# Optimization experiments

Hardware: AMD Instinct MI355X
Metric: run time of the kernel (lower is better)

The kernel has to match this reference:

```python
import jax, jax.numpy as jnp
import numpy as np

DIM = 128; DSTATE = 64; DHEAD = 64; EXPAND = 2
DINNER = EXPAND * DIM; NH = DINNER // DHEAD
CONVK = 4; CHUNK = 128
BATCH = 1; DD = 32; HH = 32; WW = 32
CONVCH = DINNER + 2 * DSTATE
DPROJ = 2 * DINNER + 2 * DSTATE + NH


def rmsnorm(v, w, eps=1e-6):
    return v * jax.lax.rsqrt(jnp.mean(v * v, axis=-1, keepdims=True) + eps) * w


def ssd(xh, dt, A, Bm, Cm):
    # chunked SSD selective scan. xh [b,l,h,p], dt [b,l,h], A [h], Bm/Cm [b,l,n]
    b, l, h, p = xh.shape
    n = Bm.shape[-1]
    c, k = l // CHUNK, CHUNK
    dA = (dt * A).reshape(b, c, k, h)
    xdt = (xh * dt[..., None]).reshape(b, c, k, h, p)
    Bm = Bm.reshape(b, c, k, n)
    Cm = Cm.reshape(b, c, k, n)
    cum = jnp.cumsum(dA, axis=2)                  # [b,c,k,h] inclusive
    cum_h = cum.transpose(0, 1, 3, 2)             # [b,c,h,k]
    tri = jnp.tril(jnp.ones((k, k), bool))
    Lmat = jnp.exp(jnp.where(tri, cum_h[..., :, None] - cum_h[..., None, :], -jnp.inf))
    CB = jnp.einsum('bctn,bcsn->bcts', Cm, Bm)
    Y_intra = jnp.einsum('bcts,bchts,bcshp->bcthp', CB, Lmat, xdt)
    decay_end = jnp.exp(cum[:, :, -1:, :] - cum)  # [b,c,k,h]
    S = jnp.einsum('bcsn,bcsh,bcshp->bchpn', Bm, decay_end, xdt)
    cdec = jnp.exp(cum[:, :, -1])                 # [b,c,h]

    def step(hprev, inp):
        s_c, dec = inp
        return dec[:, :, None, None] * hprev + s_c, hprev

    init = jnp.zeros((b, h, p, n), xh.dtype)
    _, hprevs = jax.lax.scan(step, init, (S.transpose(1, 0, 2, 3, 4), cdec.transpose(1, 0, 2)))
    hprevs = hprevs.transpose(1, 0, 2, 3, 4)      # [b,c,h,p,n] state at each chunk start
    Y_inter = jnp.einsum('bctn,bcth,bchpn->bcthp', Cm, jnp.exp(cum), hprevs)
    return (Y_intra + Y_inter).reshape(b, l, h, p)


def mamba2(x, Win, convw, convb, dtb, Alog, Dp, normw, Wout):
    b, l, _ = x.shape
    zxbcdt = x @ Win
    z = zxbcdt[..., :DINNER]
    xBC = zxbcdt[..., DINNER:DINNER + CONVCH]
    dt = zxbcdt[..., DINNER + CONVCH:]
    xc = xBC.transpose(0, 2, 1)
    xc = jax.lax.conv_general_dilated(xc, convw, (1,), [(CONVK - 1, 0)],
                                      dimension_numbers=('NCH', 'OIH', 'NCH'),
                                      feature_group_count=CONVCH)
    xBC = jax.nn.silu(xc + convb[None, :, None]).transpose(0, 2, 1)
    xh = xBC[..., :DINNER].reshape(b, l, NH, DHEAD)
    Bm = xBC[..., DINNER:DINNER + DSTATE]
    Cm = xBC[..., DINNER + DSTATE:]
    dt = jax.nn.softplus(dt + dtb)
    A = -jnp.exp(Alog)
    y = ssd(xh, dt, A, Bm, Cm) + Dp[None, None, :, None] * xh
    y = y.reshape(b, l, DINNER)
    y = rmsnorm(y * jax.nn.silu(z), normw)
    return y @ Wout


def ss3d(xn, gate_w, gate_b, ps, pn, pz):
    B, D, H, W, C = xn.shape
    x_s = xn.reshape(B, -1, C)
    x_n = jnp.transpose(xn, (0, 2, 1, 3, 4)).reshape(B, -1, C)
    x_z = jnp.transpose(xn, (0, 3, 1, 2, 4)).reshape(B, -1, C)
    o_sf = mamba2(x_s, *ps).reshape(B, D, H, W, C)
    o_sb = jnp.flip(mamba2(jnp.flip(x_s, 1), *ps), 1).reshape(B, D, H, W, C)
    o_nf = mamba2(x_n, *pn).reshape(B, H, D, W, C).transpose(0, 2, 1, 3, 4)
    o_nb = jnp.flip(mamba2(jnp.flip(x_n, 1), *pn), 1).reshape(B, H, D, W, C).transpose(0, 2, 1, 3, 4)
    o_zf = mamba2(x_z, *pz).reshape(B, W, D, H, C).transpose(0, 2, 3, 1, 4)
    o_zb = jnp.flip(mamba2(jnp.flip(x_z, 1), *pz), 1).reshape(B, W, D, H, C).transpose(0, 2, 3, 1, 4)
    stack = jnp.stack([o_sf, o_sb, o_nf, o_nb, o_zf, o_zb], axis=1)  # [B,6,D,H,W,C]
    gates = jax.nn.softmax(xn @ gate_w + gate_b, axis=-1)            # [B,D,H,W,6]
    gates = jnp.transpose(gates[..., None], (0, 4, 1, 2, 3, 5))      # [B,6,D,H,W,1]
    return (stack * gates).sum(axis=1)


def block(x, norm_w, gate_w, gate_b, ps, pn, pz, loc_dw_w, loc_dw_b, loc_pw_w, loc_pw_b,
          ca_w1, ca_b1, ca_w2, ca_b2, alpha):
    xp = jnp.transpose(x, (0, 2, 3, 4, 1))
    xn = rmsnorm(xp, norm_w)
    g = jnp.transpose(ss3d(xn, gate_w, gate_b, ps, pn, pz), (0, 4, 1, 2, 3))
    xcf = jnp.transpose(xn, (0, 4, 1, 2, 3))
    lc = jax.lax.conv_general_dilated(xcf, loc_dw_w, (1, 1, 1), [(1, 1)] * 3,
                                      dimension_numbers=('NCDHW', 'OIDHW', 'NCDHW'),
                                      feature_group_count=DIM) + loc_dw_b[None, :, None, None, None]
    lc = jax.nn.silu(jnp.einsum('bcdhw,oc->bodhw', lc, loc_pw_w) + loc_pw_b[None, :, None, None, None])
    fused = alpha * g + (1.0 - alpha) * lc
    yc = jnp.mean(fused, axis=(2, 3, 4), keepdims=True)
    yc = jnp.einsum('bcdhw,oc->bodhw', yc, ca_w1) + ca_b1[None, :, None, None, None]
    yc = jnp.where(yc >= 0, yc, 0.1 * yc)  # LeakyReLU(0.1)
    yc = jnp.einsum('bcdhw,oc->bodhw', yc, ca_w2) + ca_b2[None, :, None, None, None]
    return x + fused * jax.nn.sigmoid(yc)


def setup_inputs() -> dict:
    keys = iter(jax.random.split(jax.random.key(0), 64))

    def rn(shape, s=1.0):
        return jax.random.normal(next(keys), shape, jnp.float32) * s

    inp = {"x": rn((BATCH, DIM, DD, HH, WW))}
    inp["norm_w"] = jnp.ones((DIM,)) + rn((DIM,), 0.02)
    inp["gate_w"] = rn((DIM, 6), 0.02)
    inp["gate_b"] = jnp.zeros((6,))
    for m in ("s", "n", "zm"):
        inp[m + "_Win"] = rn((DIM, DPROJ), 0.02)
        inp[m + "_convw"] = rn((CONVCH, 1, CONVK), 0.2)
        inp[m + "_convb"] = jnp.zeros((CONVCH,))
        inp[m + "_dtb"] = rn((NH,), 0.3)
        inp[m + "_Alog"] = jnp.log(jnp.arange(1, NH + 1, dtype=jnp.float32))
        inp[m + "_D"] = jnp.ones((NH,))
        inp[m + "_normw"] = jnp.ones((DINNER,))
        inp[m + "_Wout"] = rn((DINNER, DIM), 0.02)
    inp["loc_dw_w"] = rn((DIM, 1, 3, 3, 3), 0.1)
    inp["loc_dw_b"] = jnp.zeros((DIM,))
    inp["loc_pw_w"] = rn((DIM, DIM), 0.05)
    inp["loc_pw_b"] = jnp.zeros((DIM,))
    inp["ca_w1"] = rn((DIM // 16, DIM), 0.05)
    inp["ca_b1"] = jnp.zeros((DIM // 16,))
    inp["ca_w2"] = rn((DIM, DIM // 16), 0.05)
    inp["ca_b2"] = jnp.zeros((DIM,))
    inp["alpha"] = jnp.array(0.5, jnp.float32)
    return inp


def reference(x, norm_w, gate_w, gate_b,
              s_Win, s_convw, s_convb, s_dtb, s_Alog, s_D, s_normw, s_Wout,
              n_Win, n_convw, n_convb, n_dtb, n_Alog, n_D, n_normw, n_Wout,
              zm_Win, zm_convw, zm_convb, zm_dtb, zm_Alog, zm_D, zm_normw, zm_Wout,
              loc_dw_w, loc_dw_b, loc_pw_w, loc_pw_b, ca_w1, ca_b1, ca_w2, ca_b2, alpha):
    ps = (s_Win, s_convw, s_convb, s_dtb, s_Alog, s_D, s_normw, s_Wout)
    pn = (n_Win, n_convw, n_convb, n_dtb, n_Alog, n_D, n_normw, n_Wout)
    pz = (zm_Win, zm_convw, zm_convb, zm_dtb, zm_Alog, zm_D, zm_normw, zm_Wout)
    return block(x, norm_w, gate_w, gate_b, ps, pn, pz,
                 loc_dw_w, loc_dw_b, loc_pw_w, loc_pw_b, ca_w1, ca_b1, ca_w2, ca_b2, alpha)
```

## Files before the change

### kernel.cpp

```cpp
#include <hip/hip_runtime.h>


typedef unsigned short u16;
typedef unsigned int   u32;
typedef __attribute__((ext_vector_type(8))) short short8;
typedef __attribute__((ext_vector_type(8))) _Float16 half8;
typedef __attribute__((ext_vector_type(4))) float f32x4;

#define LSEQ 32768
#define CDIM 128
#define NPROJ 644
#define ZXS 672
#define CCH 384
#define DIN 256
#define NHD 4
#define CKL 128
#define NCHK 256

__device__ __forceinline__ float b2f(u16 u){ u32 x=((u32)u)<<16; float f; __builtin_memcpy(&f,&x,4); return f; }
__device__ __forceinline__ u16 f2b(float f){ u32 x; __builtin_memcpy(&x,&f,4); x += 0x7fffu + ((x>>16)&1u); return (u16)(x>>16); }
__device__ __forceinline__ u16 f2h(float v){ _Float16 h=(_Float16)v; u16 b; __builtin_memcpy(&b,&h,2); return b; }
__device__ __forceinline__ float h2f(u16 b){ _Float16 h; __builtin_memcpy(&h,&b,2); return (float)h; }
__device__ __forceinline__ void up4(uint2 v, float* o){
  union { uint2 u; _Float16 h[4]; } c; c.u = v;
  o[0]=(float)c.h[0]; o[1]=(float)c.h[1]; o[2]=(float)c.h[2]; o[3]=(float)c.h[3];
}
__device__ __forceinline__ uint2 pk4(const float* o){
  union { uint2 u; _Float16 h[4]; } c;
  c.h[0]=(_Float16)o[0]; c.h[1]=(_Float16)o[1]; c.h[2]=(_Float16)o[2]; c.h[3]=(_Float16)o[3];
  return c.u;
}
__device__ __forceinline__ float sigmoidf_(float v){ return 1.f/(1.f+__expf(-v)); }
__device__ __forceinline__ float siluf_(float v){ return v*sigmoidf_(v); }
__device__ __forceinline__ float softplusf_(float v){ return (v>20.f)? v : log1pf(__expf(v)); }

__device__ __forceinline__ int seq2sp(int t, int run){
  int te = (run&1) ? (LSEQ-1-t) : t;
  int a = te>>10, b=(te>>5)&31, c=te&31;
  int d,h,w;
  switch(run>>1){
    case 0: d=a; h=b; w=c; break;
    case 1: h=a; d=b; w=c; break;
    default: w=a; d=b; h=c; break;
  }
  return (d<<10)|(h<<5)|w;
}

__global__ void k_xn(const float* __restrict__ x, const float* __restrict__ nw,
                     const float* __restrict__ gw, const float* __restrict__ gb,
                     float* __restrict__ XN, float* __restrict__ G){
  int s = blockIdx.x*256 + threadIdx.x;
  float ss = 0.f;
  #pragma unroll 8
  for (int c=0;c<CDIM;c++){ float v=x[c*LSEQ+s]; ss += v*v; }
  float sc = rsqrtf(ss*(1.f/CDIM)+1e-6f);
  float a[6];
  #pragma unroll
  for (int j=0;j<6;j++) a[j]=gb[j];
  #pragma unroll 8
  for (int c=0;c<CDIM;c++){
    float v = x[c*LSEQ+s]*sc*nw[c];
    XN[c*LSEQ+s] = v;
    #pragma unroll
    for (int j=0;j<6;j++) a[j] += v*gw[c*6+j];
  }
  float m=a[0];
  #pragma unroll
  for (int j=1;j<6;j++) m = fmaxf(m,a[j]);
  float e[6], ssum=0.f;
  #pragma unroll
  for (int j=0;j<6;j++){ e[j]=__expf(a[j]-m); ssum+=e[j]; }
  float inv = 1.f/ssum;
  #pragma unroll
  for (int j=0;j<6;j++) G[j*LSEQ+s] = e[j]*inv;
}

__global__ __launch_bounds__(256) void k_permprep(const float* __restrict__ XN, u16* __restrict__ XNT, int dir,
                                                  const float* __restrict__ Win, const float* __restrict__ Wout,
                                                  u16* __restrict__ WinT, u16* __restrict__ WoT){
  __shared__ u16 TS[128*34];
  int bid = blockIdx.x;
  int tid = threadIdx.x;
  if (bid < 1024){
    int a = bid>>5, b = bid&31;
    int spa = (dir==1)? b : a;
    int spb = (dir==1)? a : b;
    int spbase = spa*1024 + spb*32;
    for (int idx=tid; idx<4096; idx+=256){
      int c = idx>>5, i = idx&31;
      TS[c*34+i] = f2b(XN[c*LSEQ + spbase + i]);
    }
    __syncthreads();
    for (int idx=tid; idx<4096; idx+=256){
      int i = idx>>7, c = idx&127;
      int t = (dir==2) ? (i*1024 + a*32 + b) : (a*1024 + b*32 + i);
      XNT[t*128 + c] = TS[c*34+i];
    }
  } else if (bid < 1408){
    int idx = (bid-1024)*256 + tid;
    int j = idx>>7, k = idx&127;
    float v = (j<NPROJ)? Win[k*NPROJ + j] : 0.f;
    WinT[idx] = f2b(v);
  } else {
    int idx = (bid-1408)*256 + tid;
    int c = idx>>8, k = idx&255;
    WoT[idx] = f2h(Wout[k*CDIM + c]);
  }
}

__global__ __launch_bounds__(256) void k_gin_mfma(const u16* __restrict__ XNT, const u16* __restrict__ WinT,
                                                  u16* __restrict__ ZX, int flip){
  __shared__ u16 Asb[128*136];
  __shared__ u16 Bsb[128*136];
  int g = blockIdx.x;
  int w = (g&7)*192 + (g>>3);
  int by = w/6, bx = w - by*6;
  int j0 = bx*128, t0 = by*128;
  int tid = threadIdx.x;
  for (int ch = tid; ch < 2048; ch += 256){
    int row = ch>>4, c8 = ch&15;
    int tg = flip ? (LSEQ-1-(t0+row)) : (t0+row);
    uint4 av = *(const uint4*)(XNT + tg*128 + c8*8);
    *(uint4*)(&Asb[row*136 + c8*8]) = av;
    uint4 bv = *(const uint4*)(WinT + (j0+row)*128 + c8*8);
    *(uint4*)(&Bsb[row*136 + c8*8]) = bv;
  }
  __syncthreads();
  int lane = tid&63, wid = tid>>6;
  int wm = (wid>>1)*64, wn = (wid&1)*64;
  int lm = lane&15, lq = lane>>4;
  f32x4 acc[4][4] = {};
  for (int kt=0; kt<4; kt++){
    short8 af[4], bf[4];
    #pragma unroll
    for (int mt=0;mt<4;mt++) af[mt] = *(const short8*)(&Asb[(wm+mt*16+lm)*136 + kt*32 + lq*8]);
    #pragma unroll
    for (int nt=0;nt<4;nt++) bf[nt] = *(const short8*)(&Bsb[(wn+nt*16+lm)*136 + kt*32 + lq*8]);
    #pragma unroll
    for (int mt=0;mt<4;mt++)
      #pragma unroll
      for (int nt=0;nt<4;nt++)
        acc[mt][nt] = __builtin_amdgcn_mfma_f32_16x16x32_bf16(af[mt], bf[nt], acc[mt][nt], 0,0,0);
  }
  __syncthreads();
  #pragma unroll
  for (int mt=0;mt<4;mt++)
    #pragma unroll
    for (int nt=0;nt<4;nt++)
      #pragma unroll
      for (int r=0;r<4;r++)
        Asb[(wm+mt*16+lq*4+r)*136 + wn+nt*16+lm] = f2h(acc[mt][nt][r]);
  __syncthreads();
  if (bx < 5){
    for (int idx=tid; idx<2048; idx+=256){
      int row = idx>>4, q = idx&15;
      *(uint4*)(ZX + (t0+row)*ZXS + j0 + q*8) = *(const uint4*)(&Asb[row*136 + q*8]);
    }
  } else {
    for (int idx=tid; idx<128; idx+=256){
      *(uint2*)(ZX + (t0+idx)*ZXS + j0) = *(const uint2*)(&Asb[idx*136]);
    }
  }
}

__global__ __launch_bounds__(384) void k_convdt(const u16* __restrict__ ZX, const float* __restrict__ cw,
                                                const float* __restrict__ cb, u16* __restrict__ XB,
                                                const float* __restrict__ dtb, const float* __restrict__ Alog,
                                                float* __restrict__ DT, float* __restrict__ CUM,
                                                float* __restrict__ CDEC, float* __restrict__ DE){
  __shared__ u16 smc[35*384];
  int bid = blockIdx.x;
  int tid = threadIdx.x;
  if (bid < 1024){
    int t0 = bid*32;
    for (int idx=tid; idx<13440; idx+=384){
      int j = idx/384, chh = idx - j*384;
      int t = t0-3+j;
      smc[idx] = (t>=0)? ZX[t*ZXS + 256 + chh] : (u16)0;
    }
    __syncthreads();
    int ch = tid;
    float w0=cw[ch*4], w1=cw[ch*4+1], w2=cw[ch*4+2], w3=cw[ch*4+3], bb=cb[ch];
    for (int i=0;i<32;i++){
      float acc = w0*h2f(smc[i*384+ch]) + w1*h2f(smc[(i+1)*384+ch])
                + w2*h2f(smc[(i+2)*384+ch]) + w3*h2f(smc[(i+3)*384+ch]) + bb;
      XB[(t0+i)*CCH + ch] = f2h(siluf_(acc));
    }
  } else if (tid < 256){
    int g = (bid-1024)*4 + (tid>>6);
    int lane = tid&63;
    int c = g>>2, h = g&3;
    float A = -__expf(Alog[h]);
    float bias = dtb[h];
    int t0 = c*CKL + lane*2;
    float x0 = h2f(ZX[t0*ZXS + 640 + h]);
    float x1 = h2f(ZX[(t0+1)*ZXS + 640 + h]);
    float d0 = softplusf_(x0+bias), d1 = softplusf_(x1+bias);
    DT[t0*4+h] = d0; DT[(t0+1)*4+h] = d1;
    float e0 = d0*A, e1 = d1*A;
    float s = e0+e1;
    #pragma unroll
    for (int off=1; off<64; off<<=1){
      float v = __shfl_up(s, off, 64);
      if (lane>=off) s += v;
    }
    float c0 = s - e1, c1 = s;
    CUM[t0*4+h] = c0;
    CUM[(t0+1)*4+h] = c1;
    float tot = __shfl(s, 63, 64);
    DE[t0*4+h]     = __expf(tot - c0);
    DE[(t0+1)*4+h] = __expf(tot - c1);
    if (lane==0) CDEC[c*4+h] = __expf(tot);
  }
}

__global__ __launch_bounds__(256,4) void k_chunk(const u16* __restrict__ XB, const float* __restrict__ DT,
                                                 const float* __restrict__ CUM, const float* __restrict__ DE,
                                                 const float* __restrict__ Dp,
                                                 u16* __restrict__ YA, u16* __restrict__ ST){
  __shared__ u16 sh[19968];
  u16* R0   = sh;
  u16* Mtri = sh;
  u16* Xsh  = sh + 11264;
  u16* scr  = sh;

  int bid = blockIdx.x; int c = bid&255, h = bid>>8;
  int tid = threadIdx.x, lane = tid&63, wid = tid>>6;
  int lm = lane&15, lq = lane>>4;
  const u16* XBc = XB + c*CKL*CCH;
  const float* DTc = DT + c*CKL*4 + h;
  const float* DEc = DE + c*CKL*4 + h;

  for (int idx=tid; idx<4096; idx+=256){
    int t2 = idx>>6, n = idx&63, t = t2*2;
    const u16* r0 = XBc + t*CCH;
    float dt0 = DTc[t*4], dt1 = DTc[(t+1)*4];
    u32 xp = (u32)f2h(h2f(r0[(h<<6)+n])*dt0) | ((u32)f2h(h2f(r0[CCH+(h<<6)+n])*dt1)<<16);
    *(u32*)&Xsh[n*136 + t] = xp;
    float de0 = DEc[t*4], de1 = DEc[(t+1)*4];
    u32 bp = (u32)f2h(h2f(r0[256+n])*de0) | ((u32)f2h(h2f(r0[CCH+256+n])*de1)<<16);
    *(u32*)&R0[n*136 + t] = bp;
  }
  if (tid<128) ((float*)(Xsh + (tid>>1)*136 + 128))[tid&1] = CUM[(c*CKL+tid)*4 + h];
  __syncthreads();
  #define CUMS(t) (((const float*)(Xsh + ((t)>>1)*136 + 128))[(t)&1])

  f32x4 sa[4] = {};
  #pragma unroll
  for (int kt=0; kt<4; kt++){
    half8 aa = *(const half8*)&Xsh[(wid*16+lm)*136 + kt*32 + lq*8];
    #pragma unroll
    for (int nt=0;nt<4;nt++){
      half8 bq = *(const half8*)&R0[(nt*16+lm)*136 + kt*32 + lq*8];
      sa[nt] = __builtin_amdgcn_mfma_f32_16x16x32_f16(aa, bq, sa[nt], 0,0,0);
    }
  }
  #pragma unroll
  for (int nt=0;nt<4;nt++){
    int n = nt*16 + lm;
    #pragma unroll
    for (int r=0;r<4;r++){
      int p = wid*16 + lq*4 + r;
      ST[((c*4+h)*64 + p)*64 + n] = f2h(sa[nt][r]);
    }
  }

  int sp0 = wid, sp1 = 7 - wid;
  f32x4 cbA[4] = {};
  f32x4 cbB[8] = {};
  const u16* lanebase = XBc + lm*CCH + lq*8;
  #pragma unroll
  for (int kt=0; kt<2; kt++){
    half8 afA = *(const half8*)(lanebase + sp0*16*CCH + 320 + kt*32);
    half8 afB = *(const half8*)(lanebase + sp1*16*CCH + 320 + kt*32);
    #pragma unroll
    for (int st=0; st<8; st++){
      if (st <= sp1){
        half8 bq = *(const half8*)(lanebase + st*16*CCH + 256 + kt*32);
        if (st <= sp0)
          cbA[st&3] = __builtin_amdgcn_mfma_f32_16x16x32_f16(afA, bq, cbA[st&3], 0,0,0);
        cbB[st] = __builtin_amdgcn_mfma_f32_16x16x32_f16(afB, bq, cbB[st], 0,0,0);
      }
    }
  }
  __syncthreads();

  float dval = Dp[h];
  u16 outv[2][4][4];
  #pragma unroll
  for (int i=0;i<2;i++){
    int sp_ = i ? sp1 : sp0;
    int q = sp_ >> 1;
    int Wst = 32*q + 40;
    int mb  = 16*(32*q*q + 48*q + (sp_&1)*(32*q+40));
    u16* Mrow = Mtri + mb;
    float ct[4];
    #pragma unroll
    for (int r=0;r<4;r++) ct[r] = CUMS(sp_*16 + lq*4 + r);

    #pragma unroll
    for (int st=0; st<8; st++){
      if (st <= sp_){
        int s = st*16 + lm;
        float cs = CUMS(s);
        f32x4 cb;
        if (i==0) cb = cbA[st&3]; else cb = cbB[st];
        if (st == sp_){
          #pragma unroll
          for (int r=0;r<4;r++){
            int t = sp_*16 + lq*4 + r;
            float m = (s <= t) ? cb[r]*__expf(ct[r]-cs) : 0.f;
            Mrow[(lq*4+r)*Wst + s] = f2h(m);
          }
          if (!(sp_&1)){
            #pragma unroll
            for (int r=0;r<4;r++) Mrow[(lq*4+r)*Wst + s + 16] = 0;
          }
        } else {
          #pragma unroll
          for (int r=0;r<4;r++)
            Mrow[(lq*4+r)*Wst + s] = f2h(cb[r]*__expf(ct[r]-cs));
        }
      }
    }

    f32x4 ya[4] = {};
    int nkt = q + 1;
    #pragma unroll
    for (int kt=0; kt<4; kt++){
      if (kt < nkt){
        half8 af = *(const half8*)&Mrow[lm*Wst + kt*32 + lq*8];
        #pragma unroll
        for (int nt=0;nt<4;nt++){
          half8 bq = *(const half8*)&Xsh[(nt*16+lm)*136 + kt*32 + lq*8];
          ya[nt] = __builtin_amdgcn_mfma_f32_16x16x32_f16(af, bq, ya[nt], 0,0,0);
        }
      }
    }

    #pragma unroll
    for (int nt=0;nt<4;nt++){
      int p = nt*16 + lm;
      #pragma unroll
      for (int r=0;r<4;r++){
        int t = sp_*16 + lq*4 + r;
        float xhv = h2f(XBc[t*CCH + (h<<6) + p]);
        outv[i][nt][r] = f2h(ya[nt][r] + dval*xhv);
      }
    }
  }
  __syncthreads();

  #pragma unroll
  for (int i=0;i<2;i++){
    int sp_ = i ? sp1 : sp0;
    #pragma unroll
    for (int nt=0;nt<4;nt++)
      #pragma unroll
      for (int r=0;r<4;r++)
        scr[(sp_*16+lq*4+r)*68 + nt*16+lm] = outv[i][nt][r];
  }
  __syncthreads();
  for (int idx=tid; idx<2048; idx+=256){
    int row = idx>>4, q = idx&15;
    *(uint2*)(YA + ((c*CKL+row)<<8) + (h<<6) + q*4) = *(const uint2*)(&scr[row*68 + q*4]);
  }
  #undef CUMS
}

__global__ void k_scan(const u16* __restrict__ ST, u16* __restrict__ HP, const float* __restrict__ CDEC){
  int g = blockIdx.x*256 + threadIdx.x;
  int h = g>>12;
  float hp = 0.f;
  #pragma unroll 32
  for (int c=0;c<NCHK;c++){
    float dec = CDEC[(c<<2)+h];
    float sv = h2f(ST[g + (c<<14)]);
    HP[g + (c<<14)] = f2h(hp);
    hp = dec*hp + sv;
  }
}

__global__ __launch_bounds__(256) void k_inter(const u16* __restrict__ XB, const float* __restrict__ CUM,
                                               const u16* __restrict__ HP, u16* __restrict__ YB){
  __shared__ u16 Cs[128*72];
  __shared__ u16 Hs[4*64*72];
  __shared__ float ex_s[4*128];
  int c = blockIdx.x;
  int tid = threadIdx.x, lane = tid&63, wid = tid>>6;
  int lm = lane&15, lq = lane>>4;
  for (int idx=tid; idx<1024; idx+=256){
    int t = idx>>3, b8 = idx&7;
    *(uint4*)&Cs[t*72 + b8*8] = *(const uint4*)(XB + (c*CKL+t)*CCH + 320 + b8*8);
  }
  for (int idx=tid; idx<2048; idx+=256){
    int h = idx>>9, p = (idx>>3)&63, b8 = idx&7;
    *(uint4*)&Hs[(h*64+p)*72 + b8*8] = *(const uint4*)(HP + ((c*4+h)*64+p)*64 + b8*8);
  }
  for (int idx=tid; idx<512; idx+=256){
    int h = idx>>7, t = idx&127;
    ex_s[h*128+t] = __expf(CUM[(c*CKL+t)*4+h]);
  }
  __syncthreads();
  int h = wid;
  const u16* Hh = &Hs[h*64*72];
  f32x4 acc[8][4] = {};
  for (int kt=0; kt<2; kt++){
    half8 af[8], bfv[4];
    #pragma unroll
    for (int mt=0;mt<8;mt++) af[mt] = *(const half8*)&Cs[(mt*16+lm)*72 + kt*32 + lq*8];
    #pragma unroll
    for (int nt=0;nt<4;nt++) bfv[nt] = *(const half8*)&Hh[(nt*16+lm)*72 + kt*32 + lq*8];
    #pragma unroll
    for (int mt=0;mt<8;mt++)
      #pragma unroll
      for (int nt=0;nt<4;nt++)
        acc[mt][nt] = __builtin_amdgcn_mfma_f32_16x16x32_f16(af[mt], bfv[nt], acc[mt][nt], 0,0,0);
  }
  #pragma unroll
  for (int mt=0;mt<8;mt++){
    #pragma unroll
    for (int r=0;r<4;r++){
      int t = mt*16 + lq*4 + r;
      float e = ex_s[h*128+t];
      u16* dst = &YB[((c*CKL+t)<<8) + (h<<6)];
      #pragma unroll
      for (int nt=0;nt<4;nt++){
        int p = nt*16 + lm;
        dst[p] = f2h(e*acc[mt][nt][r]);
      }
    }
  }
}

__global__ __launch_bounds__(256) void k_gout_mfma(const u16* __restrict__ YA, const u16* __restrict__ YB,
                                                   const u16* __restrict__ ZX, const float* __restrict__ nw,
                                                   const u16* __restrict__ WoT,
                                                   const float* __restrict__ G, float* __restrict__ GACC, int run){
  __shared__ u16 Ys[128*136];
  __shared__ u16 Ws[128*136];
  __shared__ float SSs[128];
  int t0 = blockIdx.x*128;
  int tid = threadIdx.x, lane = tid&63, wid = tid>>6;
  int lm = lane&15, lq = lane>>4;
  f32x4 acc[2][8] = {};
  for (int kb=0; kb<2; kb++){
    __syncthreads();
    for (int ch=tid; ch<2048; ch+=256){
      int row = ch>>4, c8 = ch&15;
      int t = t0+row;
      int cb = kb*128 + c8*8;
      uint2 av0 = *(const uint2*)(YA + t*DIN + cb);
      uint2 av1 = *(const uint2*)(YA + t*DIN + cb + 4);
      uint2 bv0 = *(const uint2*)(YB + t*DIN + cb);
      uint2 bv1 = *(const uint2*)(YB + t*DIN + cb + 4);
      uint2 zv0 = *(const uint2*)(ZX + t*ZXS + cb);
      uint2 zv1 = *(const uint2*)(ZX + t*ZXS + cb + 4);
      float af[8], bf[8], zf[8];
      up4(av0, af); up4(av1, af+4);
      up4(bv0, bf); up4(bv1, bf+4);
      up4(zv0, zf); up4(zv1, zf+4);
      float ssp = 0.f;
      union { uint4 u; u16 h[8]; } pk;
      #pragma unroll
      for (int j=0;j<8;j++){
        float u = (af[j]+bf[j])*siluf_(zf[j]);
        ssp += u*u;
        pk.h[j] = f2h(u*nw[cb+j]);
      }
      *(uint4*)&Ys[row*136 + c8*8] = pk.u;
      *(uint4*)&Ws[row*136 + c8*8] = *(const uint4*)(WoT + row*DIN + kb*128 + c8*8);
      #pragma unroll
      for (int off=1; off<16; off<<=1) ssp += __shfl_xor(ssp, off, 64);
      if ((lane&15)==0){ if (kb==0) SSs[row] = ssp; else SSs[row] += ssp; }
    }
    __syncthreads();
    for (int kt=0; kt<4; kt++){
      half8 af[2], bfv[8];
      #pragma unroll
      for (int mt=0;mt<2;mt++) af[mt] = *(const half8*)&Ys[(wid*32+mt*16+lm)*136 + kt*32 + lq*8];
      #pragma unroll
      for (int nt=0;nt<8;nt++) bfv[nt] = *(const half8*)&Ws[(nt*16+lm)*136 + kt*32 + lq*8];
      #pragma unroll
      for (int mt=0;mt<2;mt++)
        #pragma unroll
        for (int nt=0;nt<8;nt++)
          acc[mt][nt] = __builtin_amdgcn_mfma_f32_16x16x32_f16(af[mt], bfv[nt], acc[mt][nt], 0,0,0);
    }
  }
  #pragma unroll
  for (int mt=0;mt<2;mt++){
    #pragma unroll
    for (int r=0;r<4;r++){
      int tl = wid*32 + mt*16 + lq*4 + r;
      int t = t0 + tl;
      int sp = seq2sp(t, run);
      float sc = rsqrtf(SSs[tl]*(1.f/DIN)+1e-6f);
      float g = G[run*LSEQ + sp] * sc;
      float* dst = &GACC[sp*CDIM];
      if (run==0){
        #pragma unroll
        for (int nt=0;nt<8;nt++) dst[nt*16+lm] = g*acc[mt][nt][r];
      } else {
        #pragma unroll
        for (int nt=0;nt<8;nt++) dst[nt*16+lm] += g*acc[mt][nt][r];
      }
    }
  }
}

__global__ __launch_bounds__(256) void k_dwconv(const float* __restrict__ XN, const float* __restrict__ w,
                                                const float* __restrict__ b, float* __restrict__ LC1){
  __shared__ float sm[3*34*40];
  int cc = blockIdx.x>>5, d = blockIdx.x&31;
  int tid = threadIdx.x;
  for (int i=tid; i<4080; i+=256) sm[i] = 0.f;
  __syncthreads();
  #pragma unroll
  for (int p=0;p<3;p++){
    int dz = d-1+p;
    if ((unsigned)dz<=31u){
      for (int idx=tid; idx<1024; idx+=256){
        int hh = idx>>5, ww = idx&31;
        sm[p*1360 + (hh+1)*40 + (ww+4)] = XN[cc*LSEQ + (dz<<10) + idx];
      }
    }
  }
  __syncthreads();
  float wreg[27];
  #pragma unroll
  for (int i=0;i<27;i++) wreg[i] = w[cc*27+i];
  float bias = b[cc];
  int h = tid>>3, w0 = (tid&7)*4;
  float4 acc = {bias,bias,bias,bias};
  #pragma unroll
  for (int p=0;p<3;p++){
    #pragma unroll
    for (int dy=0;dy<3;dy++){
      const float* row = &sm[p*1360 + (h+dy)*40 + 4];
      float left  = row[w0-1];
      float4 mid  = *(const float4*)&row[w0];
      float right = row[w0+4];
      float wa=wreg[p*9+dy*3+0], wb=wreg[p*9+dy*3+1], wc=wreg[p*9+dy*3+2];
      acc.x += wa*left  + wb*mid.x + wc*mid.y;
      acc.y += wa*mid.x + wb*mid.y + wc*mid.z;
      acc.z += wa*mid.y + wb*mid.z + wc*mid.w;
      acc.w += wa*mid.z + wb*mid.w + wc*right;
    }
  }
  *(float4*)&LC1[cc*LSEQ + (d<<10) + h*32 + w0] = acc;
}

__global__ __launch_bounds__(256) void k_pw(const float* __restrict__ LC1, const float* __restrict__ pw,
                                            const float* __restrict__ pwb, float* __restrict__ LC2){
  __shared__ u16 Ws[128*136];
  __shared__ u16 Bs[128*136];
  int s0 = blockIdx.x*128;
  int tid = threadIdx.x, lane = tid&63, wid = tid>>6;
  int lm = lane&15, lq = lane>>4;
  for (int idx=tid; idx<16384; idx+=256){
    int o = idx>>7, cc = idx&127;
    Ws[o*136+cc] = f2h(pw[idx]);
  }
  for (int idx=tid; idx<16384; idx+=256){
    int cc = idx>>7, n = idx&127;
    Bs[n*136+cc] = f2h(LC1[cc*LSEQ + s0 + n]);
  }
  __syncthreads();
  f32x4 acc[2][8] = {};
  for (int kt=0; kt<4; kt++){
    half8 af[2], bfv[8];
    #pragma unroll
    for (int mt=0;mt<2;mt++) af[mt] = *(const half8*)&Ws[(wid*32+mt*16+lm)*136 + kt*32 + lq*8];
    #pragma unroll
    for (int nt=0;nt<8;nt++) bfv[nt] = *(const half8*)&Bs[(nt*16+lm)*136 + kt*32 + lq*8];
    #pragma unroll
    for (int mt=0;mt<2;mt++)
      #pragma unroll
      for (int nt=0;nt<8;nt++)
        acc[mt][nt] = __builtin_amdgcn_mfma_f32_16x16x32_f16(af[mt], bfv[nt], acc[mt][nt], 0,0,0);
  }
  #pragma unroll
  for (int mt=0;mt<2;mt++){
    #pragma unroll
    for (int r=0;r<4;r++){
      int o = wid*32 + mt*16 + lq*4 + r;
      float bb = pwb[o];
      float* dst = &LC2[o*LSEQ + s0];
      #pragma unroll
      for (int nt=0;nt<8;nt++){
        int n = nt*16 + lm;
        dst[n] = siluf_(acc[mt][nt][r] + bb);
      }
    }
  }
}

__global__ void k_fuse(const float* __restrict__ GACC, const float* __restrict__ LC2,
                       const float* __restrict__ alpha, float* __restrict__ FUSED,
                       float* __restrict__ MEANP){
  __shared__ float tile[64*65];
  int bs = blockIdx.x>>1, bc = blockIdx.x&1;
  int s0 = bs*64, c0 = bc*64;
  int tid = threadIdx.x;
  float a = alpha[0];
  for (int idx=tid; idx<4096; idx+=256){
    int i = idx>>6, j = idx&63;
    tile[i*65+j] = GACC[(s0+i)*CDIM + c0+j];
  }
  __syncthreads();
  for (int idx=tid; idx<4096; idx+=256){
    int j = idx>>6, i = idx&63;
    float g = tile[i*65+j];
    float l = LC2[(c0+j)*LSEQ + s0+i];
    float f = a*g + (1.f-a)*l;
    FUSED[(c0+j)*LSEQ + s0+i] = f;
    float wsum = f;
    #pragma unroll
    for (int off=32; off; off>>=1) wsum += __shfl_xor(wsum, off, 64);
    if ((tid&63)==0) MEANP[(c0+j)*512 + bs] = wsum;
  }
}

__global__ void k_ca(const float* __restrict__ MEANP, const float* __restrict__ w1, const float* __restrict__ b1,
                     const float* __restrict__ w2, const float* __restrict__ b2, float* __restrict__ SIG){
  __shared__ float MEANsh[128];
  __shared__ float y1[8];
  int tid = threadIdx.x;
  {
    float acc = 0.f;
    const float* p = MEANP + tid*512;
    #pragma unroll 16
    for (int b=0;b<512;b++) acc += p[b];
    MEANsh[tid] = acc*(1.f/LSEQ);
  }
  __syncthreads();
  if (tid<8){
    float acc = b1[tid];
    for (int c=0;c<128;c++) acc += w1[tid*128+c]*MEANsh[c];
    y1[tid] = (acc>=0.f)? acc : 0.1f*acc;
  }
  __syncthreads();
  float acc = b2[tid];
  #pragma unroll
  for (int o=0;o<8;o++) acc += w2[tid*8+o]*y1[o];
  SIG[tid] = sigmoidf_(acc);
}

__global__ void k_final(const float* __restrict__ x, const float* __restrict__ F, const float* __restrict__ SIG,
                        float* __restrict__ out){
  int idx = blockIdx.x*256 + threadIdx.x;
  int cc = idx>>15;
  out[idx] = x[idx] + F[idx]*SIG[cc];
}

extern "C" void kernel_launch(void* const* d_in, const int* in_sizes, int n_in,
                              void* d_out, int out_size, void* d_ws, size_t ws_size,
                              hipStream_t stream){
  (void)in_sizes; (void)n_in; (void)out_size; (void)ws_size;
  const float* x       = (const float*)d_in[0];
  const float* norm_w  = (const float*)d_in[1];
  const float* gate_w  = (const float*)d_in[2];
  const float* gate_b  = (const float*)d_in[3];
  const float* loc_dw_w= (const float*)d_in[28];
  const float* loc_dw_b= (const float*)d_in[29];
  const float* loc_pw_w= (const float*)d_in[30];
  const float* loc_pw_b= (const float*)d_in[31];
  const float* ca_w1   = (const float*)d_in[32];
  const float* ca_b1   = (const float*)d_in[33];
  const float* ca_w2   = (const float*)d_in[34];
  const float* ca_b2   = (const float*)d_in[35];
  const float* alpha   = (const float*)d_in[36];

  float* W     = (float*)d_ws;
  float* XN    = W;
  float* GATES = XN    + 4194304;
  float* GACC  = GATES + 196608;
  u16*   ZX    = (u16*)(GACC + 4194304);
  u16*   XB    = (u16*)(GACC + 4194304 + 11010048);
  float* DT    = GACC + 4194304 + 11010048 + 6291456;
  float* CUM   = DT    + 131072;
  float* CDEC  = CUM   + 131072;
  float* DE    = CDEC  + 1024;
  float* STreg = DE    + 131072;
  float* Y     = STreg + 4194304;
  float* LC1   = Y     + 8388608;
  float* LC2   = LC1   + 4194304;
  float* MEANP = LC2   + 4194304;
  float* SIG   = MEANP + 65536;
  u16*   XNT   = (u16*)(SIG + 128);
  u16*   WinT  = XNT + 4194304;
  u16*   WoT   = WinT + 98304;
  u16*   ST16  = (u16*)STreg;
  u16*   YA    = (u16*)Y;
  u16*   YB    = YA + 8388608;
  u16*   HP16  = (u16*)LC1;

  k_xn<<<128,256,0,stream>>>(x, norm_w, gate_w, gate_b, XN, GATES);

  for (int r=0;r<6;r++){
    int m = r>>1;
    const float* Win   = (const float*)d_in[4 + m*8 + 0];
    const float* convw = (const float*)d_in[4 + m*8 + 1];
    const float* convb = (const float*)d_in[4 + m*8 + 2];
    const float* dtb   = (const float*)d_in[4 + m*8 + 3];
    const float* Alog  = (const float*)d_in[4 + m*8 + 4];
    const float* Dp    = (const float*)d_in[4 + m*8 + 5];
    const float* nw2   = (const float*)d_in[4 + m*8 + 6];
    const float* Wout  = (const float*)d_in[4 + m*8 + 7];
    if ((r&1)==0){
      k_permprep<<<1536,256,0,stream>>>(XN, XNT, m, Win, Wout, WinT, WoT);
    }
    k_gin_mfma<<<1536,256,0,stream>>>(XNT, WinT, ZX, r&1);
    k_convdt  <<<1280,384,0,stream>>>(ZX, convw, convb, XB, dtb, Alog, DT, CUM, CDEC, DE);
    k_chunk   <<<1024,256,0,stream>>>(XB, DT, CUM, DE, Dp, YA, ST16);
    k_scan    <<<64,256,0,stream>>>(ST16, HP16, CDEC);
    k_inter   <<<256,256,0,stream>>>(XB, CUM, HP16, YB);
    k_gout_mfma<<<256,256,0,stream>>>(YA, YB, ZX, nw2, WoT, GATES, GACC, r);
  }

  k_dwconv<<<4096,256,0,stream>>>(XN, loc_dw_w, loc_dw_b, LC1);
  k_pw    <<<256,256,0,stream>>>(LC1, loc_pw_w, loc_pw_b, LC2);
  k_fuse  <<<1024,256,0,stream>>>(GACC, LC2, alpha, LC1, MEANP);
  k_ca    <<<1,128,0,stream>>>(MEANP, ca_w1, ca_b1, ca_w2, ca_b2, SIG);
  k_final <<<16384,256,0,stream>>>(x, LC1, SIG, (float*)d_out);
}
```

Before: 942.0 us.

## Batch forward and flipped scan directions into shared chunk, scan and inter launches

```diff
diff --git a/kernel.cpp b/kernel.cpp
--- a/kernel.cpp
+++ b/kernel.cpp
@@ -10,7 +10,8 @@
 #define LSEQ 32768
 #define CDIM 128
 #define NPROJ 644
-#define ZXS 672
+#define ZVS 264
+#define XBCS 384
 #define CCH 384
 #define DIN 256
 #define NHD 4
@@ -109,7 +110,7 @@
 }
 
 __global__ __launch_bounds__(256) void k_gin_mfma(const u16* __restrict__ XNT, const u16* __restrict__ WinT,
-                                                  u16* __restrict__ ZX, int flip){
+                                                  u16* __restrict__ ZV, u16* __restrict__ ZXBC, int flip){
   __shared__ u16 Asb[128*136];
   __shared__ u16 Bsb[128*136];
   int g = blockIdx.x;
@@ -151,20 +152,26 @@
       for (int r=0;r<4;r++)
         Asb[(wm+mt*16+lq*4+r)*136 + wn+nt*16+lm] = f2h(acc[mt][nt][r]);
   __syncthreads();
-  if (bx < 5){
+  if (bx < 2){
     for (int idx=tid; idx<2048; idx+=256){
       int row = idx>>4, q = idx&15;
-      *(uint4*)(ZX + (t0+row)*ZXS + j0 + q*8) = *(const uint4*)(&Asb[row*136 + q*8]);
+      *(uint4*)(ZV + (t0+row)*ZVS + bx*128 + q*8) = *(const uint4*)(&Asb[row*136 + q*8]);
+    }
+  } else if (bx < 5){
+    for (int idx=tid; idx<2048; idx+=256){
+      int row = idx>>4, q = idx&15;
+      *(uint4*)(ZXBC + (t0+row)*XBCS + (bx-2)*128 + q*8) = *(const uint4*)(&Asb[row*136 + q*8]);
     }
   } else {
     for (int idx=tid; idx<128; idx+=256){
-      *(uint2*)(ZX + (t0+idx)*ZXS + j0) = *(const uint2*)(&Asb[idx*136]);
-    }
-  }
-}
-
-__global__ __launch_bounds__(384) void k_convdt(const u16* __restrict__ ZX, const float* __restrict__ cw,
+      *(uint2*)(ZV + (t0+idx)*ZVS + 256) = *(const uint2*)(&Asb[idx*136]);
+    }
+  }
+}
+
+__global__ __launch_bounds__(384) void k_convdt(const u16* __restrict__ ZXBC, const float* __restrict__ cw,
                                                 const float* __restrict__ cb, u16* __restrict__ XB,
+                                                const u16* __restrict__ ZV,
                                                 const float* __restrict__ dtb, const float* __restrict__ Alog,
                                                 float* __restrict__ DT, float* __restrict__ CUM,
                                                 float* __restrict__ CDEC, float* __restrict__ DE){
@@ -176,7 +183,7 @@
     for (int idx=tid; idx<13440; idx+=384){
       int j = idx/384, chh = idx - j*384;
       int t = t0-3+j;
-      smc[idx] = (t>=0)? ZX[t*ZXS + 256 + chh] : (u16)0;
+      smc[idx] = (t>=0)? ZXBC[t*XBCS + chh] : (u16)0;
     }
     __syncthreads();
     int ch = tid;
@@ -193,8 +200,8 @@
     float A = -__expf(Alog[h]);
     float bias = dtb[h];
     int t0 = c*CKL + lane*2;
-    float x0 = h2f(ZX[t0*ZXS + 640 + h]);
-    float x1 = h2f(ZX[(t0+1)*ZXS + 640 + h]);
+    float x0 = h2f(ZV[t0*ZVS + 256 + h]);
+    float x1 = h2f(ZV[(t0+1)*ZVS + 256 + h]);
     float d0 = softplusf_(x0+bias), d1 = softplusf_(x1+bias);
     DT[t0*4+h] = d0; DT[(t0+1)*4+h] = d1;
     float e0 = d0*A, e1 = d1*A;
@@ -214,17 +221,28 @@
   }
 }
 
-__global__ __launch_bounds__(256,4) void k_chunk(const u16* __restrict__ XB, const float* __restrict__ DT,
-                                                 const float* __restrict__ CUM, const float* __restrict__ DE,
+__global__ __launch_bounds__(256,4) void k_chunk(const u16* __restrict__ XB0_, const u16* __restrict__ XB1_,
+                                                 const float* __restrict__ DT0_, const float* __restrict__ DT1_,
+                                                 const float* __restrict__ CUM0_, const float* __restrict__ CUM1_,
+                                                 const float* __restrict__ DE0_, const float* __restrict__ DE1_,
                                                  const float* __restrict__ Dp,
-                                                 u16* __restrict__ YA, u16* __restrict__ ST){
+                                                 u16* __restrict__ YA0_, u16* __restrict__ YA1_,
+                                                 u16* __restrict__ ST0_, u16* __restrict__ ST1_){
   __shared__ u16 sh[19968];
   u16* R0   = sh;
   u16* Mtri = sh;
   u16* Xsh  = sh + 11264;
   u16* scr  = sh;
 
-  int bid = blockIdx.x; int c = bid&255, h = bid>>8;
+  int bid = blockIdx.x;
+  int pr = bid>>10, b = bid&1023;
+  int c = b&255, h = b>>8;
+  const u16* XB  = pr? XB1_ : XB0_;
+  const float* DT  = pr? DT1_ : DT0_;
+  const float* CUM = pr? CUM1_ : CUM0_;
+  const float* DE  = pr? DE1_ : DE0_;
+  u16* YA = pr? YA1_ : YA0_;
+  u16* ST = pr? ST1_ : ST0_;
   int tid = threadIdx.x, lane = tid&63, wid = tid>>6;
   int lm = lane&15, lq = lane>>4;
   const u16* XBc = XB + c*CKL*CCH;
@@ -368,8 +386,14 @@
   #undef CUMS
 }
 
-__global__ void k_scan(const u16* __restrict__ ST, u16* __restrict__ HP, const float* __restrict__ CDEC){
-  int g = blockIdx.x*256 + threadIdx.x;
+__global__ void k_scan(const u16* __restrict__ ST0_, const u16* __restrict__ ST1_,
+                       u16* __restrict__ HP0_, u16* __restrict__ HP1_,
+                       const float* __restrict__ CDEC0_, const float* __restrict__ CDEC1_){
+  int pr = blockIdx.x>>6;
+  const u16* ST = pr? ST1_ : ST0_;
+  u16* HP = pr? HP1_ : HP0_;
+  const float* CDEC = pr? CDEC1_ : CDEC0_;
+  int g = (blockIdx.x&63)*256 + threadIdx.x;
   int h = g>>12;
   float hp = 0.f;
   #pragma unroll 32
@@ -381,12 +405,19 @@
   }
 }
 
-__global__ __launch_bounds__(256) void k_inter(const u16* __restrict__ XB, const float* __restrict__ CUM,
-                                               const u16* __restrict__ HP, u16* __restrict__ YB){
+__global__ __launch_bounds__(256) void k_inter(const u16* __restrict__ XB0_, const u16* __restrict__ XB1_,
+                                               const float* __restrict__ CUM0_, const float* __restrict__ CUM1_,
+                                               const u16* __restrict__ HP0_, const u16* __restrict__ HP1_,
+                                               u16* __restrict__ YB0_, u16* __restrict__ YB1_){
   __shared__ u16 Cs[128*72];
   __shared__ u16 Hs[4*64*72];
   __shared__ float ex_s[4*128];
-  int c = blockIdx.x;
+  int pr = blockIdx.x>>8;
+  int c = blockIdx.x&255;
+  const u16* XB  = pr? XB1_ : XB0_;
+  const float* CUM = pr? CUM1_ : CUM0_;
+  const u16* HP  = pr? HP1_ : HP0_;
+  u16* YB = pr? YB1_ : YB0_;
   int tid = threadIdx.x, lane = tid&63, wid = tid>>6;
   int lm = lane&15, lq = lane>>4;
   for (int idx=tid; idx<1024; idx+=256){
@@ -434,7 +465,7 @@
 }
 
 __global__ __launch_bounds__(256) void k_gout_mfma(const u16* __restrict__ YA, const u16* __restrict__ YB,
-                                                   const u16* __restrict__ ZX, const float* __restrict__ nw,
+                                                   const u16* __restrict__ ZV, const float* __restrict__ nw,
                                                    const u16* __restrict__ WoT,
                                                    const float* __restrict__ G, float* __restrict__ GACC, int run){
   __shared__ u16 Ys[128*136];
@@ -454,8 +485,8 @@
       uint2 av1 = *(const uint2*)(YA + t*DIN + cb + 4);
       uint2 bv0 = *(const uint2*)(YB + t*DIN + cb);
       uint2 bv1 = *(const uint2*)(YB + t*DIN + cb + 4);
-      uint2 zv0 = *(const uint2*)(ZX + t*ZXS + cb);
-      uint2 zv1 = *(const uint2*)(ZX + t*ZXS + cb + 4);
+      uint2 zv0 = *(const uint2*)(ZV + t*ZVS + cb);
+      uint2 zv1 = *(const uint2*)(ZV + t*ZVS + cb + 4);
       float af[8], bf[8], zf[8];
       up4(av0, af); up4(av1, af+4);
       up4(bv0, bf); up4(bv1, bf+4);
@@ -674,32 +705,40 @@
 
   float* W     = (float*)d_ws;
   float* XN    = W;
-  float* GATES = XN    + 4194304;
-  float* GACC  = GATES + 196608;
-  u16*   ZX    = (u16*)(GACC + 4194304);
-  u16*   XB    = (u16*)(GACC + 4194304 + 11010048);
-  float* DT    = GACC + 4194304 + 11010048 + 6291456;
-  float* CUM   = DT    + 131072;
-  float* CDEC  = CUM   + 131072;
-  float* DE    = CDEC  + 1024;
-  float* STreg = DE    + 131072;
-  float* Y     = STreg + 4194304;
-  float* LC1   = Y     + 8388608;
-  float* LC2   = LC1   + 4194304;
-  float* MEANP = LC2   + 4194304;
-  float* SIG   = MEANP + 65536;
-  u16*   XNT   = (u16*)(SIG + 128);
-  u16*   WinT  = XNT + 4194304;
-  u16*   WoT   = WinT + 98304;
-  u16*   ST16  = (u16*)STreg;
-  u16*   YA    = (u16*)Y;
-  u16*   YB    = YA + 8388608;
-  u16*   HP16  = (u16*)LC1;
+  float* GATES = W + 4194304;
+  float* GACC  = W + 4390912;
+  u16*   XNT   = (u16*)(W + 8585216);
+  u16*   WinT  = (u16*)(W + 10682368);
+  u16*   WoT   = (u16*)(W + 10731520);
+  u16*   ZV0   = (u16*)(W + 10747904);
+  u16*   ZV1   = (u16*)(W + 15073280);
+  u16*   ZXBC  = (u16*)(W + 19398656);
+  u16*   XB0   = (u16*)(W + 25690112);
+  u16*   XB1   = (u16*)(W + 31981568);
+  float* DT0   = W + 38273024;
+  float* CUM0  = W + 38404096;
+  float* DE0   = W + 38535168;
+  float* DT1   = W + 38666240;
+  float* CUM1  = W + 38797312;
+  float* DE1   = W + 38928384;
+  float* CDEC0 = W + 39059456;
+  float* CDEC1 = W + 39060480;
+  u16*   ST0   = (u16*)(W + 39061504);
+  u16*   ST1   = ST0 + 4194304;
+  u16*   YB0   = (u16*)(W + 39061504);
+  u16*   YB1   = ZXBC;
+  u16*   YA0   = (u16*)(W + 43255808);
+  u16*   YA1   = (u16*)(W + 47450112);
+  float* LC1   = W + 51644416;
+  float* LC2   = W + 55838720;
+  float* MEANP = W + 60033024;
+  float* SIG   = W + 60098560;
+  u16*   HP0   = (u16*)LC1;
+  u16*   HP1   = (u16*)LC2;
 
   k_xn<<<128,256,0,stream>>>(x, norm_w, gate_w, gate_b, XN, GATES);
 
-  for (int r=0;r<6;r++){
-    int m = r>>1;
+  for (int m=0;m<3;m++){
     const float* Win   = (const float*)d_in[4 + m*8 + 0];
     const float* convw = (const float*)d_in[4 + m*8 + 1];
     const float* convb = (const float*)d_in[4 + m*8 + 2];
@@ -708,15 +747,18 @@
     const float* Dp    = (const float*)d_in[4 + m*8 + 5];
     const float* nw2   = (const float*)d_in[4 + m*8 + 6];
     const float* Wout  = (const float*)d_in[4 + m*8 + 7];
-    if ((r&1)==0){
-      k_permprep<<<1536,256,0,stream>>>(XN, XNT, m, Win, Wout, WinT, WoT);
-    }
-    k_gin_mfma<<<1536,256,0,stream>>>(XNT, WinT, ZX, r&1);
-    k_convdt  <<<1280,384,0,stream>>>(ZX, convw, convb, XB, dtb, Alog, DT, CUM, CDEC, DE);
-    k_chunk   <<<1024,256,0,stream>>>(XB, DT, CUM, DE, Dp, YA, ST16);
-    k_scan    <<<64,256,0,stream>>>(ST16, HP16, CDEC);
-    k_inter   <<<256,256,0,stream>>>(XB, CUM, HP16, YB);
-    k_gout_mfma<<<256,256,0,stream>>>(YA, YB, ZX, nw2, WoT, GATES, GACC, r);
+
+    k_permprep<<<1536,256,0,stream>>>(XN, XNT, m, Win, Wout, WinT, WoT);
+    k_gin_mfma<<<1536,256,0,stream>>>(XNT, WinT, ZV0, ZXBC, 0);
+    k_convdt  <<<1280,384,0,stream>>>(ZXBC, convw, convb, XB0, ZV0, dtb, Alog, DT0, CUM0, CDEC0, DE0);
+    k_gin_mfma<<<1536,256,0,stream>>>(XNT, WinT, ZV1, ZXBC, 1);
+    k_convdt  <<<1280,384,0,stream>>>(ZXBC, convw, convb, XB1, ZV1, dtb, Alog, DT1, CUM1, CDEC1, DE1);
+    k_chunk <<<2048,256,0,stream>>>(XB0, XB1, DT0, DT1, CUM0, CUM1, DE0, DE1, Dp,
+                                    YA0, YA1, ST0, ST1);
+    k_scan  <<<128,256,0,stream>>>(ST0, ST1, HP0, HP1, CDEC0, CDEC1);
+    k_inter <<<512,256,0,stream>>>(XB0, XB1, CUM0, CUM1, HP0, HP1, YB0, YB1);
+    k_gout_mfma<<<256,256,0,stream>>>(YA0, YB0, ZV0, nw2, WoT, GATES, GACC, 2*m);
+    k_gout_mfma<<<256,256,0,stream>>>(YA1, YB1, ZV1, nw2, WoT, GATES, GACC, 2*m+1);
   }
 
   k_dwconv<<<4096,256,0,stream>>>(XN, loc_dw_w, loc_dw_b, LC1);
```

Result: slower. 1.040 ms (+10.4%).

## Parallelize inter-chunk state scan by splitting chunk sequence into four segments

Applied to the files above, without the earlier changes.

```diff
diff --git a/kernel.cpp b/kernel.cpp
--- a/kernel.cpp
+++ b/kernel.cpp
@@ -368,16 +368,38 @@
   #undef CUMS
 }
 
-__global__ void k_scan(const u16* __restrict__ ST, u16* __restrict__ HP, const float* __restrict__ CDEC){
-  int g = blockIdx.x*256 + threadIdx.x;
+__global__ __launch_bounds__(256) void k_scan(const u16* __restrict__ ST, u16* __restrict__ HP,
+                                              const float* __restrict__ CDEC){
+  __shared__ float L[4][64][64];
+  __shared__ float E[4][64];
+  int tid = threadIdx.x;
+  int j = tid>>6, s = tid&63;
+  int b = blockIdx.x;
+  int g = b*64 + s;
   int h = g>>12;
-  float hp = 0.f;
-  #pragma unroll 32
-  for (int c=0;c<NCHK;c++){
-    float dec = CDEC[(c<<2)+h];
-    float sv = h2f(ST[g + (c<<14)]);
-    HP[g + (c<<14)] = f2h(hp);
-    hp = dec*hp + sv;
+  int a = j*64;
+  float hloc = 0.f;
+  #pragma unroll 16
+  for (int i=0;i<64;i++){
+    int c = a+i;
+    L[j][i][s] = hloc;
+    hloc = CDEC[(c<<2)+h]*hloc + h2f(ST[g + (c<<14)]);
+  }
+  E[j][s] = hloc;
+  __syncthreads();
+  float carry = 0.f;
+  for (int k=0;k<j;k++){
+    float P = 1.f;
+    #pragma unroll 16
+    for (int i=0;i<64;i++) P *= CDEC[((k*64+i)<<2)+h];
+    carry = E[k][s] + P*carry;
+  }
+  float m = 1.f;
+  #pragma unroll 16
+  for (int i=0;i<64;i++){
+    int c = a+i;
+    HP[g + (c<<14)] = f2h(L[j][i][s] + m*carry);
+    m *= CDEC[(c<<2)+h];
   }
 }
 
@@ -714,7 +736,7 @@
     k_gin_mfma<<<1536,256,0,stream>>>(XNT, WinT, ZX, r&1);
     k_convdt  <<<1280,384,0,stream>>>(ZX, convw, convb, XB, dtb, Alog, DT, CUM, CDEC, DE);
     k_chunk   <<<1024,256,0,stream>>>(XB, DT, CUM, DE, Dp, YA, ST16);
-    k_scan    <<<64,256,0,stream>>>(ST16, HP16, CDEC);
+    k_scan    <<<256,256,0,stream>>>(ST16, HP16, CDEC);
     k_inter   <<<256,256,0,stream>>>(XB, CUM, HP16, YB);
     k_gout_mfma<<<256,256,0,stream>>>(YA, YB, ZX, nw2, WoT, GATES, GACC, r);
   }
```

Result: faster. 910.5 us (-3.3%).
